# Kernel optimization log

Hardware: AMD Instinct MI355X
Metric: run time of the kernel (lower is better)

## Reference

```python
import jax, jax.numpy as jnp
import numpy as np

BN_EPS = 1e-5
SLOPE = 0.2  # LeakyReLU negative slope
LOCAL_POINTS = 512


def knn_idx(x, k):
    # x: [B, C, N] -> [B, N, k] indices of k nearest neighbors (incl. self)
    xx = jnp.sum(x * x, axis=1)                       # [B, N]
    inner = jnp.einsum('bcn,bcm->bnm', x, x)          # [B, N, N]
    neg_d2 = 2.0 * inner - xx[:, :, None] - xx[:, None, :]
    return jax.lax.top_k(neg_d2, k)[1]


def edge_conv(x, k, w1, b1, g, be, w2, b2):
    # EdgeConv: knn gather -> (center - neigh, center) -> 1x1 conv -> BN -> LeakyReLU -> 1x1 conv -> max over k
    B, C, N = x.shape
    idx = knn_idx(x, k)                               # [B, N, k]
    xt = jnp.transpose(x, (0, 2, 1))                  # [B, N, C]
    neigh = xt[jnp.arange(B)[:, None, None], idx]     # [B, N, k, C]
    neigh = jnp.transpose(neigh, (0, 3, 1, 2))        # [B, C, N, k]
    center = jnp.broadcast_to(x[:, :, :, None], neigh.shape)
    feat = jnp.concatenate([center - neigh, center], axis=1)  # [B, 2C, N, k]
    h = jnp.einsum('oc,bcnk->bonk', w1, feat) + b1[None, :, None, None]
    mu = jnp.mean(h, axis=(0, 2, 3), keepdims=True)   # train-mode BatchNorm2d
    var = jnp.mean((h - mu) ** 2, axis=(0, 2, 3), keepdims=True)
    h = (h - mu) / jnp.sqrt(var + BN_EPS) * g[None, :, None, None] + be[None, :, None, None]
    h = jnp.where(h >= 0, h, SLOPE * h)
    h = jnp.einsum('oc,bcnk->bonk', w2, h) + b2[None, :, None, None]
    return jnp.max(h, axis=-1)                        # [B, out, N]


def fps(xyz, m):
    # furthest point sampling; xyz: [B, N, 3] -> [B, m] int indices; starts at index 0 (CUDA convention)
    B, N, _ = xyz.shape
    idx0 = jnp.zeros((B, m), jnp.int32)
    dists0 = jnp.full((B, N), 1e10, jnp.float32)
    last0 = jnp.zeros((B,), jnp.int32)

    def body(i, carry):
        idx, dists, last = carry
        p = jnp.take_along_axis(xyz, last[:, None, None], axis=1)  # [B, 1, 3]
        d = jnp.sum((xyz - p) ** 2, axis=-1)                       # [B, N]
        dists = jnp.minimum(dists, d)
        nxt = jnp.argmax(dists, axis=1).astype(jnp.int32)
        return idx.at[:, i].set(nxt), dists, nxt

    idx, _, _ = jax.lax.fori_loop(1, m, body, (idx0, dists0, last0))
    return idx


def setup_inputs():
    key = jax.random.key(0)
    ks = jax.random.split(key, 13)
    B, N = 32, 2048
    x = jax.random.normal(ks[0], (B, 3, N), jnp.float32)

    def w(k, o, c):
        return jax.random.normal(k, (o, c), jnp.float32) * (1.0 / np.sqrt(c))

    inp = {'x': x}
    dims = [(3, 64), (64, 256), (256, 512)]
    for li, (ci, co) in enumerate(dims, start=1):
        inp[f'w{li}a'] = w(ks[4 * li - 3], co // 2, 2 * ci)
        inp[f'b{li}a'] = jnp.zeros((co // 2,), jnp.float32)
        inp[f'g{li}'] = jnp.ones((co // 2,), jnp.float32)
        inp[f'be{li}'] = jnp.zeros((co // 2,), jnp.float32)
        inp[f'w{li}b'] = w(ks[4 * li - 2], co, co // 2)
        inp[f'b{li}b'] = jnp.zeros((co,), jnp.float32)
    return inp


def reference(x, w1a, b1a, g1, be1, w1b, b1b, w2a, b2a, g2, be2, w2b, b2b, w3a, b3a, g3, be3, w3b, b3b):
    x1 = edge_conv(x, 16, w1a, b1a, g1, be1, w1b, b1b)        # [B, 64, N]
    idx = fps(jnp.transpose(x, (0, 2, 1)), LOCAL_POINTS)       # [B, M]
    x1 = jnp.take_along_axis(x1, idx[:, None, :], axis=2)      # gather_points -> [B, 64, M]
    x2 = edge_conv(x1, 8, w2a, b2a, g2, be2, w2b, b2b)         # [B, 256, M]
    x3 = edge_conv(x2, 4, w3a, b3a, g3, be3, w3b, b3b)         # [B, 512, M]
    return jnp.concatenate([x1, x2, x3], axis=1)               # [B, 832, M]
```

## Files before the change

kernel.cpp:

```cpp
#include <hip/hip_runtime.h>
#include <hip/hip_bf16.h>
#include <cstddef>


constexpr size_t OFF_IDX1 = 0;
constexpr size_t OFF_IDX2 = OFF_IDX1 + 1048576;
constexpr size_t OFF_IDX3 = OFF_IDX2 + 131072;
constexpr size_t OFF_FPS  = OFF_IDX3 + 65536;
constexpr size_t OFF_ST   = OFF_FPS + 16384;
constexpr size_t OFF_SS1  = OFF_ST + 1664;
constexpr size_t OFF_SS2  = OFF_SS1 + 64;
constexpr size_t OFF_SS3  = OFF_SS2 + 256;
constexpr size_t OFF_NORM = OFF_SS3 + 512;
constexpr size_t OFF_X1F  = OFF_NORM + 32768;

__global__ __launch_bounds__(256) void knn3d3_kernel(const float* __restrict__ x,
                                                     int* __restrict__ idx)
{
    constexpr int N = 2048, QB = 64, NS = 4, MS = N / NS , KK = 16;
    __shared__ __align__(16) double smem[5120];
    float*  sx  = (float*)smem;
    float*  sy  = sx + 2048;
    float*  sz  = sy + 2048;
    double* snd = smem + 3072;
    double* mv  = smem;
    unsigned short* mi = (unsigned short*)(smem + 4096);

    int t = threadIdx.x;
    int q = t >> 2, s = t & 3;
    int b  = blockIdx.x >> 5;
    int n0 = (blockIdx.x & 31) << 6;
    int n  = n0 + q;
    const float* xb = x + (size_t)b * 3 * N;

    for (int e = t; e < N; e += 256) {
        float mx = xb[e], my = xb[N + e], mz = xb[2 * N + e];
        sx[e] = mx; sy[e] = my; sz[e] = mz;
        double dx = (double)mx, dy = (double)my, dz = (double)mz;
        snd[e] = dx * dx + dy * dy + dz * dz;
    }
    __syncthreads();

    double qx = (double)sx[n], qy = (double)sy[n], qz = (double)sz[n];
    double qq = snd[n];
    double bv[KK]; int bi[KK];
#pragma unroll
    for (int j = 0; j < KK; ++j) { bv[j] = -1e300; bi[j] = 0; }

#pragma unroll 4
    for (int i = 0; i < MS; ++i) {
        int mm = (i + s * 8) & (MS - 1);
        int m  = s * MS + mm;
        double dot = qx * (double)sx[m] + qy * (double)sy[m] + qz * (double)sz[m];
        double val = 2.0 * dot - qq - snd[m];
        if (val > bv[KK - 1]) {
            bv[KK - 1] = val; bi[KK - 1] = m;
#pragma unroll
            for (int j = KK - 1; j > 0; --j) {
                if (bv[j] > bv[j - 1]) {
                    double tv = bv[j]; bv[j] = bv[j - 1]; bv[j - 1] = tv;
                    int    ti = bi[j]; bi[j] = bi[j - 1]; bi[j - 1] = ti;
                }
            }
        }
    }
    __syncthreads();
#pragma unroll
    for (int j = 0; j < KK; ++j) {
        mv[(q * NS + s) * KK + j] = bv[j];
        mi[(q * NS + s) * KK + j] = (unsigned short)bi[j];
    }
    __syncthreads();
    if (t < QB) {
        int qq2 = t;
        double hv[NS]; int hj[NS];
#pragma unroll
        for (int s2 = 0; s2 < NS; ++s2) { hv[s2] = mv[(qq2 * NS + s2) * KK]; hj[s2] = 0; }
        int* op = idx + ((size_t)(b * N) + n0 + qq2) * KK;
#pragma unroll
        for (int r = 0; r < KK; ++r) {
            double best = -1e301; int bs = 0;
#pragma unroll
            for (int s2 = 0; s2 < NS; ++s2) {
                if (hv[s2] > best) { best = hv[s2]; bs = s2; }
            }
#pragma unroll
            for (int s2 = 0; s2 < NS; ++s2) {
                if (s2 == bs) {
                    op[r] = (int)mi[(qq2 * NS + s2) * KK + hj[s2]];
                    hj[s2]++;
                    hv[s2] = (hj[s2] < KK) ? mv[(qq2 * NS + s2) * KK + hj[s2]] : -1e301;
                }
            }
        }
    }
}

__global__ __launch_bounds__(256) void stats1_kernel(const float* __restrict__ x,
                                                     const int* __restrict__ idx1,
                                                     const float* __restrict__ w1,
                                                     const float* __restrict__ b1,
                                                     double* __restrict__ stats)
{
    __shared__ float wl[32][9];
    __shared__ float bsh[32];
    __shared__ float red[2][4][32];
    int t = threadIdx.x;
    for (int e = t; e < 192; e += 256) wl[e / 6][e % 6] = w1[e];
    if (t < 32) bsh[t] = b1[t];
    __syncthreads();

    float sum[32], sq[32];
#pragma unroll
    for (int o = 0; o < 32; o++) { sum[o] = 0.f; sq[o] = 0.f; }

    int base = blockIdx.x * 256 + t;
    for (int it = 0; it < 16; ++it) {
        int p = base + it * 65536;
        int b = p >> 15, rem = p & 32767, n = rem >> 4;
        int m = idx1[p];
        const float* xb = x + (size_t)b * 3 * 2048;
        float cx = xb[n], cy = xb[2048 + n], cz = xb[4096 + n];
        float f0 = cx - xb[m], f1 = cy - xb[2048 + m], f2 = cz - xb[4096 + m];
#pragma unroll
        for (int o = 0; o < 32; o++) {
            float h = bsh[o] + wl[o][0] * f0 + wl[o][1] * f1 + wl[o][2] * f2
                             + wl[o][3] * cx + wl[o][4] * cy + wl[o][5] * cz;
            sum[o] += h; sq[o] += h * h;
        }
    }
    int lane = t & 63, wv = t >> 6;
#pragma unroll
    for (int o = 0; o < 32; o++) {
        float s = sum[o], q = sq[o];
#pragma unroll
        for (int d = 1; d < 64; d <<= 1) { s += __shfl_xor(s, d); q += __shfl_xor(q, d); }
        if (lane == 0) { red[0][wv][o] = s; red[1][wv][o] = q; }
    }
    __syncthreads();
    if (t < 32) {
        atomicAdd(&stats[t], (double)(red[0][0][t] + red[0][1][t] + red[0][2][t] + red[0][3][t]));
    } else if (t < 64) {
        int o = t - 32;
        atomicAdd(&stats[32 + o], (double)(red[1][0][o] + red[1][1][o] + red[1][2][o] + red[1][3][o]));
    }
}

__global__ void finalize_kernel(const double* __restrict__ stats,
                                const float* __restrict__ g,
                                const float* __restrict__ be,
                                float* __restrict__ scsh, int co2, double invcnt)
{
    int t = threadIdx.x;
    if (t < co2) {
        double mu  = stats[t] * invcnt;
        double var = stats[co2 + t] * invcnt - mu * mu;
        float  sc  = (float)((double)g[t] / sqrt(var + 1e-5));
        scsh[t]       = sc;
        scsh[co2 + t] = be[t] - (float)mu * sc;
    }
}

__global__ __launch_bounds__(256) void passB1_kernel(const float* __restrict__ x,
                                                     const int* __restrict__ idx1,
                                                     const float* __restrict__ w1,
                                                     const float* __restrict__ b1,
                                                     const float* __restrict__ scsh,
                                                     const float* __restrict__ w2,
                                                     const float* __restrict__ b2,
                                                     float* __restrict__ x1full)
{
    __shared__ float hn[256][36];
    __shared__ float wl[32][9];
    __shared__ float sc[32], sh[32], bs1[32];
    int t = threadIdx.x;
    int b = blockIdx.x >> 7, nt = blockIdx.x & 127;
    int n0 = nt << 4;
    for (int e = t; e < 192; e += 256) wl[e / 6][e % 6] = w1[e];
    if (t < 32) { sc[t] = scsh[t]; sh[t] = scsh[32 + t]; bs1[t] = b1[t]; }
    __syncthreads();
    {
        int n = n0 + (t >> 4), kk = t & 15;
        int pix = (((b << 11) + n) << 4) + kk;
        int m = idx1[pix];
        const float* xb = x + (size_t)b * 3 * 2048;
        float cx = xb[n], cy = xb[2048 + n], cz = xb[4096 + n];
        float f0 = cx - xb[m], f1 = cy - xb[2048 + m], f2 = cz - xb[4096 + m];
#pragma unroll
        for (int o = 0; o < 32; o++) {
            float h = bs1[o] + wl[o][0] * f0 + wl[o][1] * f1 + wl[o][2] * f2
                             + wl[o][3] * cx + wl[o][4] * cy + wl[o][5] * cz;
            h = h * sc[o] + sh[o];
            hn[t][o] = (h >= 0.f) ? h : 0.2f * h;
        }
    }
    __syncthreads();
    int o2 = t & 63, ng = t >> 6;
    float w2r[32];
#pragma unroll
    for (int c = 0; c < 32; c++) w2r[c] = w2[o2 * 32 + c];
    float bb = b2[o2];
#pragma unroll
    for (int ns = 0; ns < 4; ns++) {
        int nl = ng * 4 + ns;
        float mx = -1e30f;
#pragma unroll
        for (int kk = 0; kk < 16; kk++) {
            const float* hp = &hn[(nl << 4) + kk][0];
            float s = 0.f;
#pragma unroll
            for (int c4 = 0; c4 < 8; c4++) {
                float4 f = *(const float4*)(hp + c4 * 4);
                s += w2r[c4 * 4] * f.x + w2r[c4 * 4 + 1] * f.y
                   + w2r[c4 * 4 + 2] * f.z + w2r[c4 * 4 + 3] * f.w;
            }
            mx = fmaxf(mx, s);
        }
        x1full[((size_t)(b << 11) + n0 + nl) * 64 + o2] = mx + bb;
    }
}

__global__ __launch_bounds__(64) void fps_kernel(const float* __restrict__ x,
                                                 int* __restrict__ fpsidx)
{
    int b = blockIdx.x, l = threadIdx.x;
    const float* xb = x + (size_t)b * 3 * 2048;
    __shared__ float sx[2048], sy[2048], sz[2048];
    float px[32], py[32], pz[32];
    double dd[32];
#pragma unroll
    for (int j = 0; j < 32; j++) {
        int n = j * 64 + l;
        float a = xb[n], bb2 = xb[2048 + n], c = xb[4096 + n];
        px[j] = a; py[j] = bb2; pz[j] = c; dd[j] = 1e30;
        sx[n] = a; sy[n] = bb2; sz[n] = c;
    }
    __syncthreads();
    if (l == 0) fpsidx[(size_t)b * 512] = 0;
    int last = 0;
    for (int i = 1; i < 512; i++) {
        double lpx = (double)sx[last], lpy = (double)sy[last], lpz = (double)sz[last];
        double bestd = -1.0; int bestn = 0;
#pragma unroll
        for (int j = 0; j < 32; j++) {
            double dx = (double)px[j] - lpx, dy = (double)py[j] - lpy, dz = (double)pz[j] - lpz;
            double d = dx * dx + dy * dy + dz * dz;
            double nd = fmin(dd[j], d);
            dd[j] = nd;
            if (nd > bestd) { bestd = nd; bestn = j * 64 + l; }
        }
#pragma unroll
        for (int s = 1; s < 64; s <<= 1) {
            double od = __shfl_xor(bestd, s);
            int    on = __shfl_xor(bestn, s);
            if (od > bestd || (od == bestd && on < bestn)) { bestd = od; bestn = on; }
        }
        last = bestn;
        if (l == 0) fpsidx[(size_t)b * 512 + i] = bestn;
    }
}

__global__ __launch_bounds__(256) void gather_kernel(const float* __restrict__ x1full,
                                                     const int* __restrict__ fpsidx,
                                                     float* __restrict__ out)
{
    int e = blockIdx.x * 256 + threadIdx.x;
    int j = e & 511; int rest = e >> 9; int c = rest & 63; int b = rest >> 6;
    int fj = fpsidx[b * 512 + j];
    out[((size_t)b * 832 + c) * 512 + j] = x1full[((size_t)(b << 11) + fj) * 64 + c];
}

template <int C>
__global__ __launch_bounds__(256) void norms_kernel(const float* __restrict__ xin,
                                                    size_t xbstride,
                                                    double* __restrict__ norms)
{
    int b = blockIdx.x >> 1;
    int n = ((blockIdx.x & 1) << 8) + threadIdx.x;
    const float* xb = xin + (size_t)b * xbstride;
    double s = 0.0;
    for (int c = 0; c < C; c++) { double v = (double)xb[(size_t)c * 512 + n]; s += v * v; }
    norms[(b << 9) + n] = s;
}

template <int C, int KK>
__global__ __launch_bounds__(256) void knn_feat2_kernel(const float* __restrict__ xin,
                                                        size_t xbstride,
                                                        const double* __restrict__ norms,
                                                        int* __restrict__ idxout)
{
    constexpr int NN = 512, QB = 16, NS = 16, MS = NN / NS , CC = 16;
    constexpr int CHUNKS = C / CC;
    __shared__ __align__(16) double smem[4736];
    float*  sm = (float*)smem;
    float*  sq = (float*)(smem + 4096);
    double* sn = smem + 4224;
    double* mv = smem;
    int*    mi = (int*)(smem + (size_t)QB * NS * KK);

    int t = threadIdx.x;
    int q = t & 15, s = t >> 4;
    int b  = blockIdx.x >> 5;
    int n0 = (blockIdx.x & 31) << 4;
    int n  = n0 + q;
    const float* xb = xin + (size_t)b * xbstride;

    for (int e = t; e < NN; e += 256) sn[e] = norms[(b << 9) + e];

    double acc[MS];
#pragma unroll
    for (int i = 0; i < MS; ++i) acc[i] = 0.0;

    for (int ch = 0; ch < CHUNKS; ++ch) {
        int c0 = ch * CC;
        __syncthreads();
        for (int e = t; e < CC * NN; e += 256) {
            int c = e >> 9, m = e & 511;
            sm[c * NN + m] = xb[(size_t)(c0 + c) * NN + m];
        }
        {
            int c = t >> 4, qq = t & 15;
            sq[c * QB + qq] = xb[(size_t)(c0 + c) * NN + n0 + qq];
        }
        __syncthreads();
        double qv[CC];
#pragma unroll
        for (int cc = 0; cc < CC; ++cc) qv[cc] = (double)sq[cc * QB + q];
#pragma unroll
        for (int m4 = 0; m4 < MS / 4; ++m4) {
#pragma unroll
            for (int cc = 0; cc < CC; ++cc) {
                float4 f = *(const float4*)&sm[cc * NN + s * MS + m4 * 4];
                acc[m4 * 4 + 0] += qv[cc] * (double)f.x;
                acc[m4 * 4 + 1] += qv[cc] * (double)f.y;
                acc[m4 * 4 + 2] += qv[cc] * (double)f.z;
                acc[m4 * 4 + 3] += qv[cc] * (double)f.w;
            }
        }
    }

    double nq = sn[n];
    double bv[KK]; int bi[KK];
#pragma unroll
    for (int j = 0; j < KK; ++j) { bv[j] = -1e300; bi[j] = 0; }
#pragma unroll
    for (int mm = 0; mm < MS; ++mm) {
        int m = s * MS + mm;
        double val = 2.0 * acc[mm] - nq - sn[m];
        if (val > bv[KK - 1]) {
            bv[KK - 1] = val; bi[KK - 1] = m;
#pragma unroll
            for (int j = KK - 1; j > 0; --j) {
                if (bv[j] > bv[j - 1]) {
                    double tv = bv[j]; bv[j] = bv[j - 1]; bv[j - 1] = tv;
                    int    ti = bi[j]; bi[j] = bi[j - 1]; bi[j - 1] = ti;
                }
            }
        }
    }
    __syncthreads();
#pragma unroll
    for (int j = 0; j < KK; ++j) {
        mv[(q * NS + s) * KK + j] = bv[j];
        mi[(q * NS + s) * KK + j] = bi[j];
    }
    __syncthreads();
    if (t < QB) {
        int qq2 = t;
        double hv[NS]; int hj[NS];
#pragma unroll
        for (int s2 = 0; s2 < NS; ++s2) { hv[s2] = mv[(qq2 * NS + s2) * KK]; hj[s2] = 0; }
        int* op = idxout + ((size_t)(b * NN) + n0 + qq2) * KK;
#pragma unroll
        for (int r = 0; r < KK; ++r) {
            double best = -1e301; int bs = 0;
#pragma unroll
            for (int s2 = 0; s2 < NS; ++s2) {
                if (hv[s2] > best) { best = hv[s2]; bs = s2; }
            }
#pragma unroll
            for (int s2 = 0; s2 < NS; ++s2) {
                if (s2 == bs) {
                    op[r] = mi[(qq2 * NS + s2) * KK + hj[s2]];
                    hj[s2]++;
                    hv[s2] = (hj[s2] < KK) ? mv[(qq2 * NS + s2) * KK + hj[s2]] : -1e301;
                }
            }
        }
    }
}

template <int C, int CO2, bool BF16OUT>
__global__ __launch_bounds__(256) void gh_kernel(const float* __restrict__ xin,
                                                 size_t xbstride,
                                                 const float* __restrict__ w1,
                                                 const float* __restrict__ b1,
                                                 void* __restrict__ Gout,
                                                 void* __restrict__ Hout)
{
    constexpr int TN = 128, TO = 64, KC = 16, NN = 512;
    __shared__ float xs[KC][TN];
    __shared__ float wls[KC][TO];
    __shared__ float wus[KC][TO];
    int t = threadIdx.x;
    constexpr int ntiles = NN / TN, otiles = CO2 / TO;
    int bid = blockIdx.x;
    int b = bid / (ntiles * otiles);
    int rem = bid % (ntiles * otiles);
    int n0 = (rem / otiles) * TN;
    int o0 = (rem % otiles) * TO;
    const float* xb = xin + (size_t)b * xbstride;

    int tn = t & 15, to = t >> 4;
    float accG[4][8], accH[4][8];
#pragma unroll
    for (int i = 0; i < 4; i++)
#pragma unroll
        for (int j = 0; j < 8; j++) { accG[i][j] = 0.f; accH[i][j] = 0.f; }

    for (int c0 = 0; c0 < C; c0 += KC) {
        __syncthreads();
        for (int e = t; e < KC * TN; e += 256) {
            int c = e >> 7, n = e & 127;
            xs[c][n] = xb[(size_t)(c0 + c) * NN + n0 + n];
        }
        for (int e = t; e < KC * TO; e += 256) {
            int o = e >> 4, c = e & 15;
            float wl = w1[(size_t)(o0 + o) * (2 * C) + c0 + c];
            float wr = w1[(size_t)(o0 + o) * (2 * C) + C + c0 + c];
            wls[c][o] = wl;
            wus[c][o] = wl + wr;
        }
        __syncthreads();
#pragma unroll 4
        for (int c = 0; c < KC; ++c) {
            float xv[8], wlv[4], wuv[4];
#pragma unroll
            for (int j = 0; j < 8; j++) xv[j] = xs[c][tn + j * 16];
#pragma unroll
            for (int i = 0; i < 4; i++) { wlv[i] = wls[c][to + i * 16]; wuv[i] = wus[c][to + i * 16]; }
#pragma unroll
            for (int i = 0; i < 4; i++)
#pragma unroll
                for (int j = 0; j < 8; j++) {
                    accG[i][j] += wuv[i] * xv[j];
                    accH[i][j] += wlv[i] * xv[j];
                }
        }
    }
#pragma unroll
    for (int i = 0; i < 4; i++) {
        int o = o0 + to + i * 16;
        float bb = b1[o];
#pragma unroll
        for (int j = 0; j < 8; j++) {
            int n = n0 + tn + j * 16;
            size_t off = ((size_t)b * NN + n) * CO2 + o;
            if constexpr (BF16OUT) {
                ((__hip_bfloat16*)Gout)[off] = __float2bfloat16(accG[i][j] + bb);
                ((__hip_bfloat16*)Hout)[off] = __float2bfloat16(accH[i][j]);
            } else {
                ((float*)Gout)[off] = accG[i][j] + bb;
                ((float*)Hout)[off] = accH[i][j];
            }
        }
    }
}

template <int CO2, int KK, bool STATS, bool GHBF>
__global__ __launch_bounds__(CO2) void edge2_kernel(
    const void* __restrict__ Gin, const void* __restrict__ Hin,
    const int* __restrict__ idx,
    double* __restrict__ stats,
    const float* __restrict__ scsh, const float* __restrict__ w2,
    const float* __restrict__ b2,
    float* __restrict__ outp, size_t obstride, int tiles_per_block)
{
    constexpr int NN = 512, CCH = 16, TP = 32, TN = TP / KK;
    __shared__ float wtl[STATS ? 1 : CCH][STATS ? 1 : (CO2 + 1)];
    __shared__ float hn[STATS ? 1 : TP * CO2];
    __shared__ int   smidx[TP];
    int t = threadIdx.x;
    float ssum = 0.f, ssq = 0.f;

    for (int ti = 0; ti < tiles_per_block; ++ti) {
        int tileIdx = blockIdx.x * tiles_per_block + ti;
        int b = tileIdx / (NN / TN), nt = tileIdx % (NN / TN);
        int n0 = nt * TN;
        __syncthreads();
        if (t < TP) {
            int n = n0 + t / KK, kk = t % KK;
            smidx[t] = idx[((size_t)(b * NN) + n) * KK + kk];
        }
        __syncthreads();

        float h[TP];
#pragma unroll
        for (int p = 0; p < TP; p++) {
            int n = n0 + p / KK;
            int m = smidx[p];
            size_t go = ((size_t)b * NN + n) * CO2 + t;
            size_t ho = ((size_t)b * NN + m) * CO2 + t;
            float gv, hv;
            if constexpr (GHBF) {
                gv = __bfloat162float(((const __hip_bfloat16*)Gin)[go]);
                hv = __bfloat162float(((const __hip_bfloat16*)Hin)[ho]);
            } else {
                gv = ((const float*)Gin)[go];
                hv = ((const float*)Hin)[ho];
            }
            h[p] = gv - hv;
        }

        if constexpr (STATS) {
#pragma unroll
            for (int p = 0; p < TP; p++) { ssum += h[p]; ssq += h[p] * h[p]; }
        } else {
            float scv = scsh[t], shv = scsh[CO2 + t];
#pragma unroll
            for (int p = 0; p < TP; p++) {
                float v = h[p] * scv + shv;
                hn[p * CO2 + t] = (v >= 0.f) ? v : 0.2f * v;
            }
            for (int g = 0; g < 2; ++g) {
                float s[TP];
#pragma unroll
                for (int p = 0; p < TP; p++) s[p] = 0.f;
                for (int ch = 0; ch < CO2 / CCH; ++ch) {
                    int c0 = ch * CCH;
                    __syncthreads();
                    for (int e = t; e < CCH * CO2; e += CO2) {
                        int o = e / CCH, ci = e % CCH;
                        wtl[ci][o] = w2[((size_t)(g * CO2 + o)) * CO2 + c0 + ci];
                    }
                    __syncthreads();
#pragma unroll
                    for (int c4 = 0; c4 < CCH / 4; c4++) {
                        float a0 = wtl[c4 * 4][t], a1 = wtl[c4 * 4 + 1][t];
                        float a2 = wtl[c4 * 4 + 2][t], a3 = wtl[c4 * 4 + 3][t];
#pragma unroll
                        for (int p = 0; p < TP; p++) {
                            const float4 f = *(const float4*)&hn[p * CO2 + c0 + c4 * 4];
                            s[p] += a0 * f.x + a1 * f.y + a2 * f.z + a3 * f.w;
                        }
                    }
                }
                float bb2 = b2[g * CO2 + t];
#pragma unroll
                for (int nl = 0; nl < TN; ++nl) {
                    float mx = s[nl * KK];
#pragma unroll
                    for (int kk = 1; kk < KK; ++kk) mx = fmaxf(mx, s[nl * KK + kk]);
                    outp[(size_t)b * obstride + (size_t)(g * CO2 + t) * NN + n0 + nl] = mx + bb2;
                }
            }
        }
    }
    if constexpr (STATS) {
        atomicAdd(&stats[t], (double)ssum);
        atomicAdd(&stats[CO2 + t], (double)ssq);
    }
}

extern "C" void kernel_launch(void* const* d_in, const int* in_sizes, int n_in,
                              void* d_out, int out_size, void* d_ws, size_t ws_size,
                              hipStream_t stream)
{
    const float* x   = (const float*)d_in[0];
    const float* w1a = (const float*)d_in[1];
    const float* b1a = (const float*)d_in[2];
    const float* g1  = (const float*)d_in[3];
    const float* be1 = (const float*)d_in[4];
    const float* w1b = (const float*)d_in[5];
    const float* b1b = (const float*)d_in[6];
    const float* w2a = (const float*)d_in[7];
    const float* b2a = (const float*)d_in[8];
    const float* g2  = (const float*)d_in[9];
    const float* be2 = (const float*)d_in[10];
    const float* w2b = (const float*)d_in[11];
    const float* b2b = (const float*)d_in[12];
    const float* w3a = (const float*)d_in[13];
    const float* b3a = (const float*)d_in[14];
    const float* g3  = (const float*)d_in[15];
    const float* be3 = (const float*)d_in[16];
    const float* w3b = (const float*)d_in[17];
    const float* b3b = (const float*)d_in[18];

    float* out = (float*)d_out;
    float* fws = (float*)d_ws;
    int*    idx1   = (int*)(fws + OFF_IDX1);
    int*    idx2   = (int*)(fws + OFF_IDX2);
    int*    idx3   = (int*)(fws + OFF_IDX3);
    int*    fpsidx = (int*)(fws + OFF_FPS);
    double* st1 = (double*)(fws + OFF_ST);
    double* st2 = st1 + 64;
    double* st3 = st2 + 256;
    float*  ss1 = fws + OFF_SS1;
    float*  ss2 = fws + OFF_SS2;
    float*  ss3 = fws + OFF_SS3;
    double* nrm = (double*)(fws + OFF_NORM);
    float*  x1full = fws + OFF_X1F;
    float*  G2 = fws + OFF_X1F;
    float*  H2 = G2 + 2097152;
    __hip_bfloat16* G3 = (__hip_bfloat16*)(fws + OFF_X1F);
    __hip_bfloat16* H3 = (__hip_bfloat16*)(fws + OFF_X1F + 2097152);

    const size_t OB = 832 * 512;

    hipMemsetAsync(st1, 0, 832 * sizeof(double), stream);

    knn3d3_kernel<<<1024, 256, 0, stream>>>(x, idx1);
    stats1_kernel<<<256, 256, 0, stream>>>(x, idx1, w1a, b1a, st1);
    finalize_kernel<<<1, 256, 0, stream>>>(st1, g1, be1, ss1, 32, 1.0 / 1048576.0);
    passB1_kernel<<<4096, 256, 0, stream>>>(x, idx1, w1a, b1a, ss1, w1b, b1b, x1full);

    fps_kernel<<<32, 64, 0, stream>>>(x, fpsidx);
    gather_kernel<<<4096, 256, 0, stream>>>(x1full, fpsidx, out);

    norms_kernel<64><<<64, 256, 0, stream>>>(out, OB, nrm);
    knn_feat2_kernel<64, 8><<<1024, 256, 0, stream>>>(out, OB, nrm, idx2);
    gh_kernel<64, 128, false><<<256, 256, 0, stream>>>(out, OB, w2a, b2a, G2, H2);
    edge2_kernel<128, 8, true, false><<<512, 128, 0, stream>>>(
        G2, H2, idx2, st2, nullptr, nullptr, nullptr, nullptr, 0, 8);
    finalize_kernel<<<1, 256, 0, stream>>>(st2, g2, be2, ss2, 128, 1.0 / 131072.0);
    edge2_kernel<128, 8, false, false><<<4096, 128, 0, stream>>>(
        G2, H2, idx2, nullptr, ss2, w2b, b2b, out + 64 * 512, OB, 1);

    norms_kernel<256><<<64, 256, 0, stream>>>(out + 64 * 512, OB, nrm);
    knn_feat2_kernel<256, 4><<<1024, 256, 0, stream>>>(out + 64 * 512, OB, nrm, idx3);
    gh_kernel<256, 256, true><<<512, 256, 0, stream>>>(out + 64 * 512, OB, w3a, b3a, G3, H3);
    edge2_kernel<256, 4, true, true><<<512, 256, 0, stream>>>(
        G3, H3, idx3, st3, nullptr, nullptr, nullptr, nullptr, 0, 4);
    finalize_kernel<<<1, 256, 0, stream>>>(st3, g3, be3, ss3, 256, 1.0 / 65536.0);
    edge2_kernel<256, 4, false, true><<<2048, 256, 0, stream>>>(
        G3, H3, idx3, nullptr, ss3, w3b, b3b, out + 320 * 512, OB, 1);
}
```

Measured before the change: 2.633 ms.

## Spread furthest point sampling over four waves with block-level argmax reduction

The furthest-point-sampling kernel now runs 256 threads per batch instead of one 64-lane wave. Each thread holds 8 points instead of 32, and a per-iteration cross-wave reduction goes through double-buffered shared memory with one barrier. Point coordinates are packed as float4 in shared memory so the last point is read with one load. The aim is to shorten the serial 511-iteration loop, where one wave per batch did all the FP64 distance work. The cost is a __syncthreads on every iteration.

Result: faster. 2.476 ms (-6.0%).

```diff
diff --git a/kernel.cpp b/kernel.cpp
--- a/kernel.cpp
+++ b/kernel.cpp
@@ -220,43 +220,68 @@
     }
 }
 
-__global__ __launch_bounds__(64) void fps_kernel(const float* __restrict__ x,
-                                                 int* __restrict__ fpsidx)
-{
-    int b = blockIdx.x, l = threadIdx.x;
-    const float* xb = x + (size_t)b * 3 * 2048;
-    __shared__ float sx[2048], sy[2048], sz[2048];
-    float px[32], py[32], pz[32];
-    double dd[32];
-#pragma unroll
-    for (int j = 0; j < 32; j++) {
-        int n = j * 64 + l;
-        float a = xb[n], bb2 = xb[2048 + n], c = xb[4096 + n];
-        px[j] = a; py[j] = bb2; pz[j] = c; dd[j] = 1e30;
-        sx[n] = a; sy[n] = bb2; sz[n] = c;
-    }
-    __syncthreads();
-    if (l == 0) fpsidx[(size_t)b * 512] = 0;
+__global__ __launch_bounds__(256) void fps2_kernel(const float* __restrict__ x,
+                                                   int* __restrict__ fpsidx)
+{
+    constexpr int N = 2048;
+    int b = blockIdx.x, t = threadIdx.x;
+    int lane = t & 63, wv = t >> 6;
+    const float* xb = x + (size_t)b * 3 * N;
+    __shared__ __align__(16) float4 sxyz[N];
+    __shared__ double redv[2][4];
+    __shared__ int    redi[2][4];
+
+    float px[8], py[8], pz[8];
+    double dd[8];
+#pragma unroll
+    for (int j = 0; j < 8; j++) {
+        int n = j * 256 + t;
+        float a = xb[n], bb = xb[N + n], c = xb[2 * N + n];
+        px[j] = a; py[j] = bb; pz[j] = c; dd[j] = 1e10;
+        sxyz[n] = make_float4(a, bb, c, 0.f);
+    }
+    __syncthreads();
+    if (t == 0) fpsidx[(size_t)b * 512] = 0;
     int last = 0;
+
     for (int i = 1; i < 512; i++) {
-        double lpx = (double)sx[last], lpy = (double)sy[last], lpz = (double)sz[last];
-        double bestd = -1.0; int bestn = 0;
-#pragma unroll
-        for (int j = 0; j < 32; j++) {
+        float4 lp = sxyz[last];
+        double lpx = (double)lp.x, lpy = (double)lp.y, lpz = (double)lp.z;
+        double v[8];
+#pragma unroll
+        for (int j = 0; j < 8; j++) {
             double dx = (double)px[j] - lpx, dy = (double)py[j] - lpy, dz = (double)pz[j] - lpz;
             double d = dx * dx + dy * dy + dz * dz;
             double nd = fmin(dd[j], d);
-            dd[j] = nd;
-            if (nd > bestd) { bestd = nd; bestn = j * 64 + l; }
-        }
+            dd[j] = nd; v[j] = nd;
+        }
+        double a0 = v[0], a1 = v[1], a2 = v[2], a3 = v[3];
+        int    i0 = t,    i1 = 256 + t, i2 = 512 + t, i3 = 768 + t;
+        if (v[4] > a0) { a0 = v[4]; i0 = 1024 + t; }
+        if (v[5] > a1) { a1 = v[5]; i1 = 1280 + t; }
+        if (v[6] > a2) { a2 = v[6]; i2 = 1536 + t; }
+        if (v[7] > a3) { a3 = v[7]; i3 = 1792 + t; }
+        if (a2 > a0) { a0 = a2; i0 = i2; }
+        if (a3 > a1) { a1 = a3; i1 = i3; }
+        if (a1 > a0) { a0 = a1; i0 = i1; }
+        double bestd = a0; int bestn = i0;
 #pragma unroll
         for (int s = 1; s < 64; s <<= 1) {
             double od = __shfl_xor(bestd, s);
             int    on = __shfl_xor(bestn, s);
             if (od > bestd || (od == bestd && on < bestn)) { bestd = od; bestn = on; }
         }
-        last = bestn;
-        if (l == 0) fpsidx[(size_t)b * 512 + i] = bestn;
+        int buf = i & 1;
+        if (lane == 0) { redv[buf][wv] = bestd; redi[buf][wv] = bestn; }
+        __syncthreads();
+        double fb = redv[buf][0]; int fn = redi[buf][0];
+#pragma unroll
+        for (int w2 = 1; w2 < 4; w2++) {
+            double ov = redv[buf][w2]; int on = redi[buf][w2];
+            if (ov > fb || (ov == fb && on < fn)) { fb = ov; fn = on; }
+        }
+        last = fn;
+        if (t == 0) fpsidx[(size_t)b * 512 + i] = fn;
     }
 }
 
@@ -614,7 +639,7 @@
     finalize_kernel<<<1, 256, 0, stream>>>(st1, g1, be1, ss1, 32, 1.0 / 1048576.0);
     passB1_kernel<<<4096, 256, 0, stream>>>(x, idx1, w1a, b1a, ss1, w1b, b1b, x1full);
 
-    fps_kernel<<<32, 64, 0, stream>>>(x, fpsidx);
+    fps2_kernel<<<32, 256, 0, stream>>>(x, fpsidx);
     gather_kernel<<<4096, 256, 0, stream>>>(x1full, fpsidx, out);
 
     norms_kernel<64><<<64, 256, 0, stream>>>(out, OB, nrm);
```
